# Kernel tuning notes

Hardware: AMD Instinct MI355X
Metric: run time of the kernel (lower is better)

## Reference

```python
import jax, jax.numpy as jnp
import numpy as np

B, S, H, E, C, V = 512, 256, 768, 6, 10, 3


def setup_inputs() -> dict:
    key = jax.random.key(0)
    ks = jax.random.split(key, 16)

    def w(k, shape):
        fan_in = shape[-1]
        return jax.random.normal(k, shape, dtype=jnp.float32) / np.sqrt(fan_in)

    return {
        'x': jax.random.randint(ks[0], (B, S), 0, V, dtype=jnp.int64),
        'emb': w(ks[1], (V, E)),
        'W_fx': w(ks[2], (H, E)), 'W_fh': w(ks[3], (H, H)), 'b_f': w(ks[4], (H, 1)),
        'W_ix': w(ks[5], (H, E)), 'W_ih': w(ks[6], (H, H)), 'b_i': w(ks[7], (H, 1)),
        'W_ox': w(ks[8], (H, E)), 'W_oh': w(ks[9], (H, H)), 'b_o': w(ks[10], (H, 1)),
        'W_cx': w(ks[11], (H, E)), 'b_c': w(ks[12], (H, 1)),
        'W_ph': w(ks[13], (C, H)), 'b_p': w(ks[14], (C, 1)),
        'c_init': jax.random.normal(ks[15], (H, B), dtype=jnp.float32) / np.sqrt(B),
    }


def reference(x, emb, W_fx, W_fh, b_f, W_ix, W_ih, b_i, W_ox, W_oh, b_o,
              W_cx, b_c, W_ph, b_p, c_init):
    # Embed tokens: [B, S] -> [B, S, E] -> time-major [S, E, B]
    xe = jnp.transpose(emb[x], (1, 2, 0))
    xs = xe[: S - 1]  # loop runs seq_length - 1 steps

    def step(carry, x_t):
        c_prev, _ = carry  # c_prev: [H, B], x_t: [E, B]
        f_t = jax.nn.sigmoid(W_fx @ x_t + W_fh @ c_prev + b_f)
        i_t = jax.nn.sigmoid(W_ix @ x_t + W_ih @ c_prev + b_i)
        o_t = jax.nn.sigmoid(W_ox @ x_t + W_oh @ c_prev + b_o)
        c_t = jax.nn.sigmoid(W_cx @ x_t + b_c) * i_t + c_prev * f_t
        h_t = jnp.tanh(c_t) * o_t
        return (c_t, h_t), None

    h0 = jnp.zeros((H, B), dtype=c_init.dtype)
    (c_fin, h_fin), _ = jax.lax.scan(step, (c_init, h0), xs)
    p_t = W_ph @ h_fin + b_p  # [C, B]
    return jax.nn.log_softmax(p_t.T, axis=-1)  # [B, C]
```

## Files before the change

kernel.cpp:

```cpp
#include <hip/hip_runtime.h>


typedef _Float16 f16x8 __attribute__((ext_vector_type(8)));
typedef _Float16 f16x4 __attribute__((ext_vector_type(4)));
typedef float    f32x4 __attribute__((ext_vector_type(4)));

#define Hdim  768
#define Bdim  512
#define Sdim  256
#define NSTEP 255
#define Edim  6
#define NCls  10
#define NGRP  16
#define NRB   12
#define GC    32
#define HB    64
#define NKK   24
#define NK2   12
#define CSTR  776
#define XSTR  260
#define ZSTR  33
#define PLANE (Bdim * Hdim)
#define SCL      4096.0f
#define SCL_INV  2.44140625e-4f

#define WP_FRAGS   (2 * NRB * 4 * NKK * 64)
#define WS_CBUF    0u
#define WS_HFIN    (2u * 2u * PLANE * 2u)
#define WS_BAR     (WS_HFIN + Bdim * Hdim * 4u)
#define WS_WPK     (WS_BAR + 4096u)
#define WS_BAR_BYTES (NGRP * 16u * 4u)

__device__ __forceinline__ float sigf(float z) { return 1.0f / (1.0f + __expf(-z)); }

__device__ __forceinline__ f32x4 mf(f16x8 a, f16x8 b, f32x4 c) {
    return __builtin_amdgcn_mfma_f32_16x16x32_f16(a, b, c, 0, 0, 0);
}

__device__ __forceinline__ void keepalive(f16x8& x) {
    asm volatile("" : "+v"(x));
}

__global__ void __launch_bounds__(256)
prep_w(const float* __restrict__ Wfh, const float* __restrict__ Wih,
       _Float16* __restrict__ wpk)
{
    const int fid  = blockIdx.x * 256 + threadIdx.x;
    const int lane = fid & 63;
    const int t1   = fid >> 6;
    const int kk   = t1 % NKK;
    const int gi   = t1 / NKK;
    const int sub  = gi & 3;
    const int t3   = gi >> 2;
    const int rb   = t3 % NRB;
    const int gate = t3 / NRB;
    const int q = lane >> 4, r = lane & 15;
    const int row = rb * 64 + sub * 16 + r;
    const int col = kk * 32 + q * 8;
    const float* src = (gate ? Wih : Wfh) + (size_t)row * Hdim + col;
    f16x8 hi, lo;
    #pragma unroll
    for (int j = 0; j < 8; ++j) {
        const float v = src[j];
        const _Float16 h = (_Float16)v;
        hi[j] = h;
        lo[j] = (_Float16)((v - (float)h) * SCL);
    }
    *(f16x8*)&wpk[(size_t)fid * 8] = hi;
    *(f16x8*)&wpk[((size_t)WP_FRAGS + fid) * 8] = lo;
}

__global__ void __launch_bounds__(512, 1)
lstm_persist(const int* __restrict__ xk, const float* __restrict__ emb,
             const float* __restrict__ Wfx, const float* __restrict__ bfv,
             const float* __restrict__ Wix, const float* __restrict__ biv,
             const float* __restrict__ Wox, const float* __restrict__ Woh,
             const float* __restrict__ bov,
             const float* __restrict__ Wcx, const float* __restrict__ bcv,
             const float* __restrict__ cinit,
             const _Float16* __restrict__ wpk,
             _Float16* __restrict__ cbuf, float* __restrict__ hfin,
             unsigned int* __restrict__ bar)
{
    __shared__ __align__(16) _Float16 ldsH[GC * CSTR];
    __shared__ __align__(16) _Float16 ldsM[GC * CSTR];
    __shared__ __align__(16) float    tbl[3 * HB * 4];
    __shared__ __align__(16) float    zred[4 * 4 * 64 * 4];
    __shared__ __align__(16) float    zbufP[2 * HB * ZSTR];
    __shared__ __align__(4)  unsigned char xtok[GC * XSTR];
    __shared__ int s_flag;

    const int tid  = threadIdx.x;
    const int w    = tid >> 6;
    const int lane = tid & 63;
    const int q    = lane >> 4;
    const int r    = lane & 15;
    const int kh   = w & 1;
    const int pr   = w >> 1;
    const int gt   = pr >> 1;
    const int rh   = pr & 1;
    const int subp = rh * 2 + kh;
    const int bid  = blockIdx.x;
    const int g    = bid & 15;
    const int rb   = bid >> 4;
    const int blkh0 = rb * HB;
    const int gc0   = g * GC;
    const int hq0   = blkh0 + subp * 16 + q * 4;

    if (tid == 0) s_flag = 0;
    __syncthreads();
    if (tid < 256) {
        if (xk[(size_t)gc0 * Sdim + 2 * tid + 1] != 0) s_flag = 1;
    }
    if (tid < 3 * HB) {
        const int v  = tid >> 6;
        const int hl = tid & 63;
        const int hg = blkh0 + hl;
        float pf = bfv[hg], pi = biv[hg], po = bov[hg], pc = bcv[hg];
        #pragma unroll
        for (int e = 0; e < Edim; ++e) {
            const float ev = emb[v * Edim + e];
            pf += Wfx[hg * Edim + e] * ev;
            pi += Wix[hg * Edim + e] * ev;
            po += Wox[hg * Edim + e] * ev;
            pc += Wcx[hg * Edim + e] * ev;
        }
        float* t = &tbl[(v * HB + hl) * 4];
        t[0] = pf; t[1] = pi; t[2] = po; t[3] = sigf(pc);
    }
    __syncthreads();
    const int is64 = (s_flag == 0);

    {
        const int col   = tid >> 4;
        const int sbase = (tid & 15) * 16;
        const size_t rowb = (size_t)(gc0 + col) * Sdim;
        for (int k2 = 0; k2 < 16; ++k2) {
            const int s0 = sbase + k2;
            const size_t idx = rowb + s0;
            xtok[col * XSTR + s0] = (unsigned char)xk[is64 ? (idx << 1) : idx];
        }
    }

    f16x8 whi[2][NK2], wlo[2][NK2];
    #pragma unroll
    for (int s2 = 0; s2 < 2; ++s2) {
        const int gis = (gt * NRB + rb) * 4 + (rh * 2 + s2);
        #pragma unroll
        for (int k2 = 0; k2 < NK2; ++k2) {
            const size_t fo = ((size_t)(gis * NKK + kh * NK2 + k2) * 64 + lane) * 8;
            whi[s2][k2] = *(const f16x8*)&wpk[fo];
            wlo[s2][k2] = *(const f16x8*)&wpk[(size_t)WP_FRAGS * 8 + fo];
        }
    }
    #pragma unroll
    for (int s2 = 0; s2 < 2; ++s2)
        #pragma unroll
        for (int k2 = 0; k2 < NK2; ++k2) {
            keepalive(whi[s2][k2]);
            keepalive(wlo[s2][k2]);
        }

    float cst[2][4];
    #pragma unroll
    for (int ct = 0; ct < 2; ++ct) {
        const int b = gc0 + ct * 16 + r;
        #pragma unroll
        for (int reg = 0; reg < 4; ++reg)
            cst[ct][reg] = cinit[(size_t)(hq0 + reg) * Bdim + b];
    }

    for (int i = 0; i < 48; ++i) {
        const int idx = tid + i * 512;
        const int col = idx & 31, k = idx >> 5;
        const float v = cinit[(size_t)k * Bdim + gc0 + col];
        const _Float16 h = (_Float16)v;
        ldsH[col * CSTR + k] = h;
        ldsM[col * CSTR + k] = (_Float16)((v - (float)h) * SCL);
    }

    for (int s = 0; s < NSTEP; ++s) {
        __syncthreads();

        f32x4 ah0c0 = {0,0,0,0}, ax0c0 = {0,0,0,0}, ah0c1 = {0,0,0,0}, ax0c1 = {0,0,0,0};
        f32x4 ah1c0 = {0,0,0,0}, ax1c0 = {0,0,0,0}, ah1c1 = {0,0,0,0}, ax1c1 = {0,0,0,0};
        #pragma unroll
        for (int k2 = 0; k2 < NK2; ++k2) {
            const int lo = (kh * NK2 + k2) * 32 + q * 8;
            const f16x8 bh0 = *(const f16x8*)&ldsH[ r       * CSTR + lo];
            const f16x8 bm0 = *(const f16x8*)&ldsM[ r       * CSTR + lo];
            const f16x8 bh1 = *(const f16x8*)&ldsH[(16 + r) * CSTR + lo];
            const f16x8 bm1 = *(const f16x8*)&ldsM[(16 + r) * CSTR + lo];
            ah0c0 = mf(whi[0][k2], bh0, ah0c0);
            ax0c0 = mf(whi[0][k2], bm0, ax0c0);
            ax0c0 = mf(wlo[0][k2], bh0, ax0c0);
            ah1c0 = mf(whi[1][k2], bh0, ah1c0);
            ax1c0 = mf(whi[1][k2], bm0, ax1c0);
            ax1c0 = mf(wlo[1][k2], bh0, ax1c0);
            ah0c1 = mf(whi[0][k2], bh1, ah0c1);
            ax0c1 = mf(whi[0][k2], bm1, ax0c1);
            ax0c1 = mf(wlo[0][k2], bh1, ax0c1);
            ah1c1 = mf(whi[1][k2], bh1, ah1c1);
            ax1c1 = mf(whi[1][k2], bm1, ax1c1);
            ax1c1 = mf(wlo[1][k2], bh1, ax1c1);
        }

        if (gt == 0) {
            const f32x4 sH0 = kh ? ah0c0 : ah1c0;
            const f32x4 sX0 = kh ? ax0c0 : ax1c0;
            const f32x4 sH1 = kh ? ah0c1 : ah1c1;
            const f32x4 sX1 = kh ? ax0c1 : ax1c1;
            f32x4* zr = (f32x4*)zred;
            zr[(w * 4 + 0) * 64 + lane] = sH0;
            zr[(w * 4 + 1) * 64 + lane] = sX0;
            zr[(w * 4 + 2) * 64 + lane] = sH1;
            zr[(w * 4 + 3) * 64 + lane] = sX1;
        } else {
            float* zp = &zbufP[kh * (HB * ZSTR)];
            #pragma unroll
            for (int s2 = 0; s2 < 2; ++s2) {
                const f32x4 h0 = s2 ? ah1c0 : ah0c0;
                const f32x4 x0 = s2 ? ax1c0 : ax0c0;
                const f32x4 h1 = s2 ? ah1c1 : ah0c1;
                const f32x4 x1 = s2 ? ax1c1 : ax0c1;
                #pragma unroll
                for (int reg = 0; reg < 4; ++reg) {
                    const int row = rh * 32 + s2 * 16 + q * 4 + reg;
                    zp[row * ZSTR + r]      = h0[reg] + x0[reg] * SCL_INV;
                    zp[row * ZSTR + 16 + r] = h1[reg] + x1[reg] * SCL_INV;
                }
            }
        }
        __syncthreads();

        if (gt == 0) {
            const f32x4* zr = (const f32x4*)zred;
            const int pw = w ^ 1;
            const f32x4 pH0 = zr[(pw * 4 + 0) * 64 + lane];
            const f32x4 pX0 = zr[(pw * 4 + 1) * 64 + lane];
            const f32x4 pH1 = zr[(pw * 4 + 2) * 64 + lane];
            const f32x4 pX1 = zr[(pw * 4 + 3) * 64 + lane];
            const f32x4 kH0 = kh ? ah1c0 : ah0c0;
            const f32x4 kX0 = kh ? ax1c0 : ax0c0;
            const f32x4 kH1 = kh ? ah1c1 : ah0c1;
            const f32x4 kX1 = kh ? ax1c1 : ax0c1;
            float zf[2][4];
            #pragma unroll
            for (int reg = 0; reg < 4; ++reg) {
                zf[0][reg] = (kH0[reg] + pH0[reg]) + (kX0[reg] + pX0[reg]) * SCL_INV;
                zf[1][reg] = (kH1[reg] + pH1[reg]) + (kX1[reg] + pX1[reg]) * SCL_INV;
            }
            const int rowl0 = rh * 32 + kh * 16 + q * 4;

            if (s != NSTEP - 1) {
                _Float16* cwH = cbuf + (size_t)(((s + 1) & 1) * 2) * PLANE;
                _Float16* cwM = cwH + PLANE;
                #pragma unroll
                for (int ct = 0; ct < 2; ++ct) {
                    const int bl = ct * 16 + r;
                    const int v  = xtok[bl * XSTR + s];
                    const float* tb = &tbl[(v * HB + subp * 16 + q * 4) * 4];
                    f16x4 cvh, cvm;
                    #pragma unroll
                    for (int reg = 0; reg < 4; ++reg) {
                        const int rowl = rowl0 + reg;
                        const float zi = zbufP[rowl * ZSTR + bl]
                                       + zbufP[HB * ZSTR + rowl * ZSTR + bl];
                        const float* tt = tb + reg * 4;
                        const float fg = sigf(zf[ct][reg] + tt[0]);
                        const float ig = sigf(zi + tt[1]);
                        const float cn = tt[3] * ig + cst[ct][reg] * fg;
                        cst[ct][reg] = cn;
                        const _Float16 ch = (_Float16)cn;
                        cvh[reg] = ch;
                        cvm[reg] = (_Float16)((cn - (float)ch) * SCL);
                    }
                    unsigned long long uh, um;
                    __builtin_memcpy(&uh, &cvh, 8);
                    __builtin_memcpy(&um, &cvm, 8);
                    const size_t eo = (size_t)(gc0 + bl) * Hdim + hq0;
                    __hip_atomic_store((unsigned long long*)&cwH[eo], uh,
                                       __ATOMIC_RELAXED, __HIP_MEMORY_SCOPE_AGENT);
                    __hip_atomic_store((unsigned long long*)&cwM[eo], um,
                                       __ATOMIC_RELAXED, __HIP_MEMORY_SCOPE_AGENT);
                }
            } else {
                f32x4 o0h = {0,0,0,0}, o0x = {0,0,0,0}, o1h = {0,0,0,0}, o1x = {0,0,0,0};
                const int arow = blkh0 + subp * 16 + r;
                #pragma unroll
                for (int kk = 0; kk < NKK; ++kk) {
                    const float* wp = Woh + (size_t)arow * Hdim + kk * 32 + q * 8;
                    f16x8 who;
                    #pragma unroll
                    for (int j = 0; j < 8; ++j) who[j] = (_Float16)wp[j];
                    const int lo = kk * 32 + q * 8;
                    const f16x8 bh0 = *(const f16x8*)&ldsH[ r       * CSTR + lo];
                    const f16x8 bm0 = *(const f16x8*)&ldsM[ r       * CSTR + lo];
                    const f16x8 bh1 = *(const f16x8*)&ldsH[(16 + r) * CSTR + lo];
                    const f16x8 bm1 = *(const f16x8*)&ldsM[(16 + r) * CSTR + lo];
                    o0h = mf(who, bh0, o0h);  o0x = mf(who, bm0, o0x);
                    o1h = mf(who, bh1, o1h);  o1x = mf(who, bm1, o1x);
                }
                #pragma unroll
                for (int ct = 0; ct < 2; ++ct) {
                    const int bl = ct * 16 + r;
                    const int v  = xtok[bl * XSTR + s];
                    const float* tb = &tbl[(v * HB + subp * 16 + q * 4) * 4];
                    const f32x4 zoh = ct ? o1h : o0h;
                    const f32x4 zox = ct ? o1x : o0x;
                    f32x4 hv;
                    #pragma unroll
                    for (int reg = 0; reg < 4; ++reg) {
                        const int rowl = rowl0 + reg;
                        const float zi = zbufP[rowl * ZSTR + bl]
                                       + zbufP[HB * ZSTR + rowl * ZSTR + bl];
                        const float zo = zoh[reg] + zox[reg] * SCL_INV;
                        const float* tt = tb + reg * 4;
                        const float fg = sigf(zf[ct][reg] + tt[0]);
                        const float ig = sigf(zi + tt[1]);
                        const float og = sigf(zo + tt[2]);
                        const float cn = tt[3] * ig + cst[ct][reg] * fg;
                        const float e  = __expf(-2.0f * fabsf(cn));
                        const float th = __builtin_copysignf((1.0f - e) / (1.0f + e), cn);
                        hv[reg] = th * og;
                    }
                    *(f32x4*)&hfin[(size_t)(gc0 + bl) * Hdim + hq0] = hv;
                }
            }
        }

        if (s < NSTEP - 1) {
            asm volatile("s_waitcnt vmcnt(0)" ::: "memory");
            __syncthreads();
            if (w == 0) {
                if (lane == 0)
                    __hip_atomic_store(&bar[g * 16 + rb], (unsigned)(s + 1),
                                       __ATOMIC_RELAXED, __HIP_MEMORY_SCOPE_AGENT);
                const unsigned tgt = (unsigned)(s + 1);
                while (true) {
                    unsigned vv = tgt;
                    if (lane < NRB)
                        vv = __hip_atomic_load(&bar[g * 16 + lane],
                                               __ATOMIC_RELAXED, __HIP_MEMORY_SCOPE_AGENT);
                    if (__all(vv >= tgt)) break;
                    __builtin_amdgcn_s_sleep(2);
                }
            }
            __syncthreads();
            const _Float16* crH = cbuf + (size_t)(((s + 1) & 1) * 2) * PLANE;
            const _Float16* crM = crH + PLANE;
            const int col = tid >> 4, j = tid & 15;
            const size_t rowo = (size_t)(gc0 + col) * Hdim;
            {
                unsigned long long th[12];
                #pragma unroll
                for (int i = 0; i < 12; ++i)
                    th[i] = __hip_atomic_load((unsigned long long*)&crH[rowo + (j + 16 * i) * 4],
                                              __ATOMIC_RELAXED, __HIP_MEMORY_SCOPE_AGENT);
                #pragma unroll
                for (int i = 0; i < 12; ++i)
                    *(unsigned long long*)&ldsH[col * CSTR + (j + 16 * i) * 4] = th[i];
            }
            {
                unsigned long long tm[12];
                #pragma unroll
                for (int i = 0; i < 12; ++i)
                    tm[i] = __hip_atomic_load((unsigned long long*)&crM[rowo + (j + 16 * i) * 4],
                                              __ATOMIC_RELAXED, __HIP_MEMORY_SCOPE_AGENT);
                #pragma unroll
                for (int i = 0; i < 12; ++i)
                    *(unsigned long long*)&ldsM[col * CSTR + (j + 16 * i) * 4] = tm[i];
            }
        }
    }
}

__global__ void __launch_bounds__(64)
proj_kernel(const float* __restrict__ hfin, const float* __restrict__ Wph,
            const float* __restrict__ bpv, float* __restrict__ out)
{
    const int b = blockIdx.x;
    const int lane = threadIdx.x;
    float acc[NCls];
    #pragma unroll
    for (int c = 0; c < NCls; ++c) acc[c] = 0.f;
    const float* hb = &hfin[(size_t)b * Hdim];
    for (int i = 0; i < Hdim / 64; ++i) {
        const float hv = hb[lane + i * 64];
        #pragma unroll
        for (int c = 0; c < NCls; ++c)
            acc[c] += Wph[c * Hdim + lane + i * 64] * hv;
    }
    #pragma unroll
    for (int c = 0; c < NCls; ++c) {
        float v = acc[c];
        #pragma unroll
        for (int off = 32; off > 0; off >>= 1)
            v += __shfl_xor(v, off, 64);
        acc[c] = v + bpv[c];
    }
    float m = acc[0];
    #pragma unroll
    for (int c = 1; c < NCls; ++c) m = fmaxf(m, acc[c]);
    float ssum = 0.f;
    #pragma unroll
    for (int c = 0; c < NCls; ++c) ssum += __expf(acc[c] - m);
    const float lse = m + __logf(ssum);
    if (lane < NCls) out[b * NCls + lane] = acc[lane] - lse;
}

extern "C" void kernel_launch(void* const* d_in, const int* in_sizes, int n_in,
                              void* d_out, int out_size, void* d_ws, size_t ws_size,
                              hipStream_t stream)
{
    const int*   xk    = (const int*)d_in[0];
    const float* emb   = (const float*)d_in[1];
    const float* Wfx   = (const float*)d_in[2];
    const float* Wfh   = (const float*)d_in[3];
    const float* bfv   = (const float*)d_in[4];
    const float* Wix   = (const float*)d_in[5];
    const float* Wih   = (const float*)d_in[6];
    const float* biv   = (const float*)d_in[7];
    const float* Wox   = (const float*)d_in[8];
    const float* Woh   = (const float*)d_in[9];
    const float* bov   = (const float*)d_in[10];
    const float* Wcx   = (const float*)d_in[11];
    const float* bcv   = (const float*)d_in[12];
    const float* Wph   = (const float*)d_in[13];
    const float* bpv   = (const float*)d_in[14];
    const float* cinit = (const float*)d_in[15];

    char* ws = (char*)d_ws;
    _Float16*     cbuf = (_Float16*)(ws + WS_CBUF);
    float*        hfin = (float*)(ws + WS_HFIN);
    unsigned int* bar  = (unsigned int*)(ws + WS_BAR);
    _Float16*     wpk  = (_Float16*)(ws + WS_WPK);

    hipMemsetAsync(bar, 0, WS_BAR_BYTES, stream);

    prep_w<<<dim3(WP_FRAGS / 256), dim3(256), 0, stream>>>(Wfh, Wih, wpk);

    lstm_persist<<<dim3(NGRP * NRB), dim3(512), 0, stream>>>(
        xk, emb, Wfx, bfv, Wix, biv, Wox, Woh, bov, Wcx, bcv,
        cinit, wpk, cbuf, hfin, bar);

    proj_kernel<<<dim3(Bdim), dim3(64), 0, stream>>>(hfin, Wph, bpv, (float*)d_out);
}
```

Measured before the change: 2.121 ms.

## Spread gate epilogue across all waves via shared z buffers and LDS cell state

Both gate groups now write their partial pre-activations to shared-memory buffers (zbufF, zbufP), and the cell state moves from registers into LDS. This lets all 8 waves run the per-step sigmoid, cell update and fp16 hi/lo store instead of only the 4 gt==0 waves. The aim is to shorten the serial epilogue on the recurrence's critical path, at the cost of extra LDS traffic and a different global store pattern.

After: 2.370 ms. 11.7% more time.

```diff
diff --git a/kernel.cpp b/kernel.cpp
--- a/kernel.cpp
+++ b/kernel.cpp
@@ -85,8 +85,9 @@
     __shared__ __align__(16) _Float16 ldsH[GC * CSTR];
     __shared__ __align__(16) _Float16 ldsM[GC * CSTR];
     __shared__ __align__(16) float    tbl[3 * HB * 4];
-    __shared__ __align__(16) float    zred[4 * 4 * 64 * 4];
+    __shared__ __align__(16) float    zbufF[2 * HB * ZSTR];
     __shared__ __align__(16) float    zbufP[2 * HB * ZSTR];
+    __shared__ __align__(16) float    cstL[HB * ZSTR];
     __shared__ __align__(4)  unsigned char xtok[GC * XSTR];
     __shared__ int s_flag;
 
@@ -161,13 +162,11 @@
             keepalive(wlo[s2][k2]);
         }
 
-    float cst[2][4];
-    #pragma unroll
-    for (int ct = 0; ct < 2; ++ct) {
-        const int b = gc0 + ct * 16 + r;
-        #pragma unroll
-        for (int reg = 0; reg < 4; ++reg)
-            cst[ct][reg] = cinit[(size_t)(hq0 + reg) * Bdim + b];
+    for (int i = 0; i < 4; ++i) {
+        const int idx = tid + i * 512;
+        const int row = idx >> 5, col = idx & 31;
+        cstL[row * ZSTR + col] =
+            cinit[(size_t)(blkh0 + row) * Bdim + gc0 + col];
     }
 
     for (int i = 0; i < 48; ++i) {
@@ -205,18 +204,8 @@
             ax1c1 = mf(wlo[1][k2], bh1, ax1c1);
         }
 
-        if (gt == 0) {
-            const f32x4 sH0 = kh ? ah0c0 : ah1c0;
-            const f32x4 sX0 = kh ? ax0c0 : ax1c0;
-            const f32x4 sH1 = kh ? ah0c1 : ah1c1;
-            const f32x4 sX1 = kh ? ax0c1 : ax1c1;
-            f32x4* zr = (f32x4*)zred;
-            zr[(w * 4 + 0) * 64 + lane] = sH0;
-            zr[(w * 4 + 1) * 64 + lane] = sX0;
-            zr[(w * 4 + 2) * 64 + lane] = sH1;
-            zr[(w * 4 + 3) * 64 + lane] = sX1;
-        } else {
-            float* zp = &zbufP[kh * (HB * ZSTR)];
+        {
+            float* zp = (gt == 0 ? zbufF : zbufP) + kh * (HB * ZSTR);
             #pragma unroll
             for (int s2 = 0; s2 < 2; ++s2) {
                 const f32x4 h0 = s2 ? ah1c0 : ah0c0;
@@ -233,99 +222,83 @@
         }
         __syncthreads();
 
-        if (gt == 0) {
-            const f32x4* zr = (const f32x4*)zred;
-            const int pw = w ^ 1;
-            const f32x4 pH0 = zr[(pw * 4 + 0) * 64 + lane];
-            const f32x4 pX0 = zr[(pw * 4 + 1) * 64 + lane];
-            const f32x4 pH1 = zr[(pw * 4 + 2) * 64 + lane];
-            const f32x4 pX1 = zr[(pw * 4 + 3) * 64 + lane];
-            const f32x4 kH0 = kh ? ah1c0 : ah0c0;
-            const f32x4 kX0 = kh ? ax1c0 : ax0c0;
-            const f32x4 kH1 = kh ? ah1c1 : ah0c1;
-            const f32x4 kX1 = kh ? ax1c1 : ax0c1;
-            float zf[2][4];
+        if (s != NSTEP - 1) {
+            const int ecol = lane & 31;
+            const int h2   = lane >> 5;
+            const int row0 = w * 8 + h2 * 4;
+            const int v    = xtok[ecol * XSTR + s];
+            const float* tb = &tbl[(v * HB + row0) * 4];
+            _Float16* cwH = cbuf + (size_t)(((s + 1) & 1) * 2) * PLANE;
+            _Float16* cwM = cwH + PLANE;
+            f16x4 cvh, cvm;
             #pragma unroll
             for (int reg = 0; reg < 4; ++reg) {
-                zf[0][reg] = (kH0[reg] + pH0[reg]) + (kX0[reg] + pX0[reg]) * SCL_INV;
-                zf[1][reg] = (kH1[reg] + pH1[reg]) + (kX1[reg] + pX1[reg]) * SCL_INV;
-            }
-            const int rowl0 = rh * 32 + kh * 16 + q * 4;
-
-            if (s != NSTEP - 1) {
-                _Float16* cwH = cbuf + (size_t)(((s + 1) & 1) * 2) * PLANE;
-                _Float16* cwM = cwH + PLANE;
-                #pragma unroll
-                for (int ct = 0; ct < 2; ++ct) {
-                    const int bl = ct * 16 + r;
-                    const int v  = xtok[bl * XSTR + s];
-                    const float* tb = &tbl[(v * HB + subp * 16 + q * 4) * 4];
-                    f16x4 cvh, cvm;
-                    #pragma unroll
-                    for (int reg = 0; reg < 4; ++reg) {
-                        const int rowl = rowl0 + reg;
-                        const float zi = zbufP[rowl * ZSTR + bl]
-                                       + zbufP[HB * ZSTR + rowl * ZSTR + bl];
-                        const float* tt = tb + reg * 4;
-                        const float fg = sigf(zf[ct][reg] + tt[0]);
-                        const float ig = sigf(zi + tt[1]);
-                        const float cn = tt[3] * ig + cst[ct][reg] * fg;
-                        cst[ct][reg] = cn;
-                        const _Float16 ch = (_Float16)cn;
-                        cvh[reg] = ch;
-                        cvm[reg] = (_Float16)((cn - (float)ch) * SCL);
-                    }
-                    unsigned long long uh, um;
-                    __builtin_memcpy(&uh, &cvh, 8);
-                    __builtin_memcpy(&um, &cvm, 8);
-                    const size_t eo = (size_t)(gc0 + bl) * Hdim + hq0;
-                    __hip_atomic_store((unsigned long long*)&cwH[eo], uh,
-                                       __ATOMIC_RELAXED, __HIP_MEMORY_SCOPE_AGENT);
-                    __hip_atomic_store((unsigned long long*)&cwM[eo], um,
-                                       __ATOMIC_RELAXED, __HIP_MEMORY_SCOPE_AGENT);
+                const int rowl = row0 + reg;
+                const float zfv = zbufF[rowl * ZSTR + ecol]
+                                + zbufF[HB * ZSTR + rowl * ZSTR + ecol];
+                const float ziv = zbufP[rowl * ZSTR + ecol]
+                                + zbufP[HB * ZSTR + rowl * ZSTR + ecol];
+                const float* tt = tb + reg * 4;
+                const float fg = sigf(zfv + tt[0]);
+                const float ig = sigf(ziv + tt[1]);
+                const float cn = tt[3] * ig + cstL[rowl * ZSTR + ecol] * fg;
+                cstL[rowl * ZSTR + ecol] = cn;
+                const _Float16 ch = (_Float16)cn;
+                cvh[reg] = ch;
+                cvm[reg] = (_Float16)((cn - (float)ch) * SCL);
+            }
+            unsigned long long uh, um;
+            __builtin_memcpy(&uh, &cvh, 8);
+            __builtin_memcpy(&um, &cvm, 8);
+            const size_t eo = (size_t)(gc0 + ecol) * Hdim + blkh0 + row0;
+            __hip_atomic_store((unsigned long long*)&cwH[eo], uh,
+                               __ATOMIC_RELAXED, __HIP_MEMORY_SCOPE_AGENT);
+            __hip_atomic_store((unsigned long long*)&cwM[eo], um,
+                               __ATOMIC_RELAXED, __HIP_MEMORY_SCOPE_AGENT);
+        } else if (gt == 0) {
+            f32x4 o0h = {0,0,0,0}, o0x = {0,0,0,0}, o1h = {0,0,0,0}, o1x = {0,0,0,0};
+            const int arow = blkh0 + subp * 16 + r;
+            #pragma unroll
+            for (int kk = 0; kk < NKK; ++kk) {
+                const float* wp = Woh + (size_t)arow * Hdim + kk * 32 + q * 8;
+                f16x8 who;
+                #pragma unroll
+                for (int j = 0; j < 8; ++j) who[j] = (_Float16)wp[j];
+                const int lo = kk * 32 + q * 8;
+                const f16x8 bh0 = *(const f16x8*)&ldsH[ r       * CSTR + lo];
+                const f16x8 bm0 = *(const f16x8*)&ldsM[ r       * CSTR + lo];
+                const f16x8 bh1 = *(const f16x8*)&ldsH[(16 + r) * CSTR + lo];
+                const f16x8 bm1 = *(const f16x8*)&ldsM[(16 + r) * CSTR + lo];
+                o0h = mf(who, bh0, o0h);  o0x = mf(who, bm0, o0x);
+                o1h = mf(who, bh1, o1h);  o1x = mf(who, bm1, o1x);
+            }
+            const int rowl0 = subp * 16 + q * 4;
+            #pragma unroll
+            for (int ct = 0; ct < 2; ++ct) {
+                const int bl = ct * 16 + r;
+                const int v  = xtok[bl * XSTR + s];
+                const float* tb = &tbl[(v * HB + rowl0) * 4];
+                const f32x4 zoh = ct ? o1h : o0h;
+                const f32x4 zox = ct ? o1x : o0x;
+                f32x4 hv;
+                #pragma unroll
+                for (int reg = 0; reg < 4; ++reg) {
+                    const int rowl = rowl0 + reg;
+                    const float zfv = zbufF[rowl * ZSTR + bl]
+                                    + zbufF[HB * ZSTR + rowl * ZSTR + bl];
+                    const float ziv = zbufP[rowl * ZSTR + bl]
+                                    + zbufP[HB * ZSTR + rowl * ZSTR + bl];
+                    const float zo = zoh[reg] + zox[reg] * SCL_INV;
+                    const float* tt = tb + reg * 4;
+                    const float fg = sigf(zfv + tt[0]);
+                    const float ig = sigf(ziv + tt[1]);
+                    const float og = sigf(zo + tt[2]);
+                    const float cn = tt[3] * ig + cstL[rowl * ZSTR + bl] * fg;
+                    const float e  = __expf(-2.0f * fabsf(cn));
+                    const float th = __builtin_copysignf((1.0f - e) / (1.0f + e), cn);
+                    hv[reg] = th * og;
                 }
-            } else {
-                f32x4 o0h = {0,0,0,0}, o0x = {0,0,0,0}, o1h = {0,0,0,0}, o1x = {0,0,0,0};
-                const int arow = blkh0 + subp * 16 + r;
-                #pragma unroll
-                for (int kk = 0; kk < NKK; ++kk) {
-                    const float* wp = Woh + (size_t)arow * Hdim + kk * 32 + q * 8;
-                    f16x8 who;
-                    #pragma unroll
-                    for (int j = 0; j < 8; ++j) who[j] = (_Float16)wp[j];
-                    const int lo = kk * 32 + q * 8;
-                    const f16x8 bh0 = *(const f16x8*)&ldsH[ r       * CSTR + lo];
-                    const f16x8 bm0 = *(const f16x8*)&ldsM[ r       * CSTR + lo];
-                    const f16x8 bh1 = *(const f16x8*)&ldsH[(16 + r) * CSTR + lo];
-                    const f16x8 bm1 = *(const f16x8*)&ldsM[(16 + r) * CSTR + lo];
-                    o0h = mf(who, bh0, o0h);  o0x = mf(who, bm0, o0x);
-                    o1h = mf(who, bh1, o1h);  o1x = mf(who, bm1, o1x);
-                }
-                #pragma unroll
-                for (int ct = 0; ct < 2; ++ct) {
-                    const int bl = ct * 16 + r;
-                    const int v  = xtok[bl * XSTR + s];
-                    const float* tb = &tbl[(v * HB + subp * 16 + q * 4) * 4];
-                    const f32x4 zoh = ct ? o1h : o0h;
-                    const f32x4 zox = ct ? o1x : o0x;
-                    f32x4 hv;
-                    #pragma unroll
-                    for (int reg = 0; reg < 4; ++reg) {
-                        const int rowl = rowl0 + reg;
-                        const float zi = zbufP[rowl * ZSTR + bl]
-                                       + zbufP[HB * ZSTR + rowl * ZSTR + bl];
-                        const float zo = zoh[reg] + zox[reg] * SCL_INV;
-                        const float* tt = tb + reg * 4;
-                        const float fg = sigf(zf[ct][reg] + tt[0]);
-                        const float ig = sigf(zi + tt[1]);
-                        const float og = sigf(zo + tt[2]);
-                        const float cn = tt[3] * ig + cst[ct][reg] * fg;
-                        const float e  = __expf(-2.0f * fabsf(cn));
-                        const float th = __builtin_copysignf((1.0f - e) / (1.0f + e), cn);
-                        hv[reg] = th * og;
-                    }
-                    *(f32x4*)&hfin[(size_t)(gc0 + bl) * Hdim + hq0] = hv;
-                }
+                *(f32x4*)&hfin[(size_t)(gc0 + bl) * Hdim + hq0] = hv;
             }
         }
 
```
